# Performance work log

Hardware: AMD Instinct MI355X
Metric: run time of the kernel (lower is better)

## Reference

```python
import jax, jax.numpy as jnp
import numpy as np

N_STATE = 32  # SSM states per channel (S4D)


def lrelu(x):
    return jnp.where(x >= 0, x, 0.3 * x)


def conv1d(x, w, b, stride=1, pad=0, dil=1):
    # x: [B,C,L], w: [O,I,K]
    y = jax.lax.conv_general_dilated(
        x, w, (stride,), [(pad, pad)], rhs_dilation=(dil,),
        dimension_numbers=('NCH', 'OIH', 'NCH'))
    return y + b[None, :, None]


def batchnorm(x, g, b, eps=1e-5):
    # training-mode BatchNorm1d: stats over (B, L) per channel
    m = jnp.mean(x, axis=(0, 2), keepdims=True)
    v = jnp.var(x, axis=(0, 2), keepdims=True)
    return (x - m) * jax.lax.rsqrt(v + eps) * g[None, :, None] + b[None, :, None]


def s4_layer(u, log_dt, C2, D):
    # Diagonal S4 (S4D-Lin): u [B,H,L] -> y [B,H,L]; causal FFT conv + skip
    H, N = C2.shape[0], C2.shape[1]
    L = u.shape[-1]
    A = -0.5 + 1j * jnp.pi * jnp.arange(N, dtype=jnp.float32)            # [N]
    dtA = jnp.exp(log_dt)[:, None] * A[None, :]                          # [H,N]
    C = (C2[..., 0] + 1j * C2[..., 1]) * (jnp.exp(dtA) - 1.0) / A        # [H,N]
    vand = jnp.exp(dtA[:, :, None] * jnp.arange(L, dtype=jnp.float32))   # [H,N,L]
    K = 2.0 * jnp.real(jnp.einsum('hn,hnl->hl', C, vand))                # [H,L]
    uf = jnp.fft.rfft(u, n=2 * L)
    Kf = jnp.fft.rfft(K, n=2 * L)
    y = jnp.fft.irfft(uf * Kf[None], n=2 * L)[..., :L]
    return y + D[None, :, None] * u


def down_block(x, s4p, convs, g, b):
    # dilated residual inception down block: S4 then 4 stride-4 dilated convs
    x = s4_layer(x, *s4p)
    d1 = batchnorm(conv1d(x, convs[0][0], convs[0][1], 4, 1, 1), g, b)
    d2 = batchnorm(lrelu(conv1d(x, convs[1][0], convs[1][1], 4, 2, 2)), g, b)
    d3 = batchnorm(lrelu(conv1d(x, convs[2][0], convs[2][1], 4, 4, 4)), g, b)
    d4 = batchnorm(lrelu(conv1d(x, convs[3][0], convs[3][1], 4, 8, 8)), g, b)
    return jnp.concatenate([d1, d2, d3, d4], axis=1)


def setup_inputs() -> dict:
    key = jax.random.key(0)
    ks = iter(jax.random.split(key, 64))

    def nrm(shape, scale=1.0):
        return jax.random.normal(next(ks), shape, jnp.float32) * scale

    def logdt(H):
        lo, hi = np.log(0.001), np.log(0.1)
        return jax.random.uniform(next(ks), (H,), jnp.float32) * (hi - lo) + lo

    B, L, DIN = 16, 8192, 2
    inp = {}
    inp['x'] = nrm((B, L, DIN))
    inp['enc_w'] = nrm((64, DIN, 1), (1.0 / DIN) ** 0.5)
    inp['enc_b'] = jnp.zeros((64,), jnp.float32)
    for pfx, H in (('s4a', 64), ('s4b', 256), ('s4c', 1024)):
        inp[pfx + '_log_dt'] = logdt(H)
        inp[pfx + '_C'] = nrm((H, N_STATE, 2), 0.5 ** 0.5)
        inp[pfx + '_D'] = nrm((H,))
    for blk, C in (('b1', 64), ('b2', 256)):
        sc = (1.0 / (C * 3)) ** 0.5
        for i in range(1, 5):
            inp[f'{blk}_w{i}'] = nrm((C, C, 3), sc)
            inp[f'{blk}_b{i}'] = nrm((C,), 0.02)
    inp['bn1_g'] = jnp.ones((64,), jnp.float32)
    inp['bn1_b'] = jnp.zeros((64,), jnp.float32)
    inp['bn2_g'] = jnp.ones((256,), jnp.float32)
    inp['bn2_b'] = jnp.zeros((256,), jnp.float32)
    inp['dec1_w'] = nrm((256, 1024, 1), (1.0 / 1024) ** 0.5)
    inp['dec1_b'] = jnp.zeros((256,), jnp.float32)
    inp['dec2_w'] = nrm((1, 256, 1), (1.0 / 256) ** 0.5)
    inp['dec2_b'] = jnp.zeros((1,), jnp.float32)
    return inp


def reference(x, enc_w, enc_b,
              s4a_log_dt, s4a_C, s4a_D,
              b1_w1, b1_b1, b1_w2, b1_b2, b1_w3, b1_b3, b1_w4, b1_b4, bn1_g, bn1_b,
              s4b_log_dt, s4b_C, s4b_D,
              b2_w1, b2_b1, b2_w2, b2_b2, b2_w3, b2_b3, b2_w4, b2_b4, bn2_g, bn2_b,
              s4c_log_dt, s4c_C, s4c_D,
              dec1_w, dec1_b, dec2_w, dec2_b):
    h = conv1d(jnp.transpose(x, (0, 2, 1)), enc_w, enc_b)                 # [B,64,L]
    x1 = down_block(h, (s4a_log_dt, s4a_C, s4a_D),
                    [(b1_w1, b1_b1), (b1_w2, b1_b2), (b1_w3, b1_b3), (b1_w4, b1_b4)],
                    bn1_g, bn1_b)                                          # [B,256,L/4]
    x2 = down_block(x1, (s4b_log_dt, s4b_C, s4b_D),
                    [(b2_w1, b2_b1), (b2_w2, b2_b2), (b2_w3, b2_b3), (b2_w4, b2_b4)],
                    bn2_g, bn2_b)                                          # [B,1024,L/16]
    x3 = s4_layer(x2, s4c_log_dt, s4c_C, s4c_D)
    y = conv1d(conv1d(x3, dec1_w, dec1_b), dec2_w, dec2_b)                 # [B,1,L/16]
    ff = jnp.squeeze(y, axis=1)                                            # [B,L/16]
    return ff[..., -1:]                                                    # [B,1]
```

## Files before the change

kernel.cpp:

```cpp
#include <hip/hip_runtime.h>
#include <math.h>

#define PI_F 3.14159265358979323846f

typedef __attribute__((ext_vector_type(8))) short short8;
typedef __attribute__((ext_vector_type(4))) float f32x4;

__device__ __forceinline__ unsigned short f2bf(float f) {
    unsigned int u = __float_as_uint(f);
    unsigned int r = (u + 0x7fffu + ((u >> 16) & 1u)) >> 16;
    return (unsigned short)r;
}
__device__ __forceinline__ float bf2f(unsigned short v) {
    return __uint_as_float((unsigned int)v << 16);
}

__global__ __launch_bounds__(128) void prep_all(
    const float* __restrict__ ldt_a, const float* __restrict__ C2_a,
    const float* __restrict__ Dv_a,
    unsigned short* __restrict__ TA_a, unsigned short* __restrict__ VA_a,
    float* __restrict__ rs_a, float* __restrict__ Vrs_a,
    const float* __restrict__ ldt_b, const float* __restrict__ C2_b,
    const float* __restrict__ Dv_b,
    unsigned short* __restrict__ TA_b, unsigned short* __restrict__ VA_b,
    float* __restrict__ rs_b, float* __restrict__ Vrs_b,
    const float* __restrict__ w0, const float* __restrict__ w1,
    const float* __restrict__ w2, const float* __restrict__ w3,
    const float* __restrict__ w4, const float* __restrict__ w5,
    const float* __restrict__ w6, const float* __restrict__ w7,
    unsigned short* __restrict__ wprep)
{
    int bid = blockIdx.x, t = threadIdx.x;
    if (bid >= 320) {
        const float* wsrc[8] = {w0, w1, w2, w3, w4, w5, w6, w7};
        int e0 = (bid - 320) * 256 + t;
#pragma unroll
        for (int half = 0; half < 2; half++) {
            int e = e0 + half * 128;
            if (e < 835584) {
                int id; int doff; int Cin;
                if (e < 49152) { id = e / 12288; doff = id * 12288; Cin = 64; }
                else { id = 4 + (e - 49152) / 196608; doff = 49152 + (id - 4) * 196608; Cin = 256; }
                int el = e - doff;
                int kb = el / (Cin * 32);
                int rem = el - kb * (Cin * 32);
                int o = rem >> 5, kk = rem & 31;
                int cch = kb / 6, t6 = kb % 6, k = t6 >> 1, chalf = t6 & 1;
                int c = cch * 64 + chalf * 32 + kk;
                wprep[e] = f2bf(wsrc[id][((size_t)o * Cin + c) * 3 + k]);
            }
        }
        return;
    }
    const float* log_dt; const float* C2; const float* Dv;
    unsigned short* TA; unsigned short* VA; float* rs; float* Vrs; int h;
    if (bid < 64) { h = bid;      log_dt = ldt_a; C2 = C2_a; Dv = Dv_a; TA = TA_a; VA = VA_a; rs = rs_a; Vrs = Vrs_a; }
    else          { h = bid - 64; log_dt = ldt_b; C2 = C2_b; Dv = Dv_b; TA = TA_b; VA = VA_b; rs = rs_b; Vrs = Vrs_b; }
    __shared__ float cn[64];
    __shared__ float sK[128];
    __shared__ unsigned short s_w[128 * 66];
    float dt = expf(log_dt[h]);
    if (t < 32) {
        int n = t;
        float e = expf(-0.5f*dt);
        float s_, c_; sincosf(PI_F*dt*n, &s_, &c_);
        float wr = e*c_, wi = e*s_;
        float ar = -0.5f, ai = PI_F*n;
        float den = 1.f/(ar*ar + ai*ai);
        float tr = wr - 1.f, ti = wi;
        float qr = (tr*ar + ti*ai)*den;
        float qi = (ti*ar - tr*ai)*den;
        float c2r = C2[((size_t)h*32+n)*2], c2i = C2[((size_t)h*32+n)*2+1];
        cn[2*n]   = 2.f*(c2r*qr - c2i*qi);
        cn[2*n+1] = 2.f*(c2r*qi + c2i*qr);
        float e128 = expf(-64.f*dt);
        float s2, c2v; sincosf(PI_F*dt*n*128.f, &s2, &c2v);
        float pr = 1.f - e128*c2v, pim = -e128*s2;
        float dr = 1.f - wr, di = -wi;
        float dd = 1.f/(dr*dr + di*di);
        Vrs[(size_t)h*64 + 2*n]   = (pr*dr + pim*di)*dd;
        Vrs[(size_t)h*64 + 2*n+1] = (pim*dr - pr*di)*dd;
    }
    __syncthreads();
    {
        float em = expf(-0.5f*dt*t);
        float Kt = 0.f;
        for (int n = 0; n < 32; n++) {
            float s_, c_; sincosf(PI_F*dt*(float)(n*t), &s_, &c_);
            Kt += cn[2*n]*em*c_ - cn[2*n+1]*em*s_;
        }
        sK[t] = Kt + (t == 0 ? Dv[h] : 0.f);
    }
    if (t < 64) {
        int n = t >> 1, ri = t & 1;
        float e = expf(-0.5f*dt);
        float s_, c_; sincosf(PI_F*dt*n, &s_, &c_);
        float wr = e*c_, wi = e*s_;
        float crn = cn[2*n], cin = cn[2*n+1];
        float pr = wr, pim = wi;
        for (int m = 0; m < 128; m++) {
            float re = crn*pr - cin*pim;
            float im = crn*pim + cin*pr;
            s_w[m*66 + t] = f2bf(ri ? -im : re);
            float nr = pr*wr - pim*wi;
            float ni = pr*wi + pim*wr;
            pr = nr; pim = ni;
        }
    } else {
        int r = t - 64; int n = r >> 1, ri = r & 1;
        float e = expf(-0.5f*dt);
        float s_, c_; sincosf(PI_F*dt*n, &s_, &c_);
        float wr = e*c_, wi = e*s_;
        float cr2 = 1.f, ci2 = 0.f;
        for (int kb = 3; kb >= 0; kb--) {
            unsigned short buf[32];
            for (int kk = 31; kk >= 0; kk--) {
                buf[kk] = f2bf(ri ? ci2 : cr2);
                float nr = cr2*wr - ci2*wi;
                float ni = cr2*wi + ci2*wr;
                cr2 = nr; ci2 = ni;
            }
            uint4* dst = (uint4*)&VA[(((size_t)h*4 + kb)*64 + r)*32];
            uint4* src = (uint4*)buf;
            dst[0]=src[0]; dst[1]=src[1]; dst[2]=src[2]; dst[3]=src[3];
        }
    }
    __syncthreads();
    {
        float acc = 0.f;
        for (int tau = 0; tau <= t; tau++) acc += sK[tau];
        rs[(size_t)h*128 + t] = acc;
    }
    for (int kb = 0; kb < 4; kb++) {
        unsigned short tb[32];
#pragma unroll
        for (int kk = 0; kk < 32; kk++) {
            int col = kb*32 + kk;
            tb[kk] = f2bf((col <= t) ? sK[t - col] : 0.f);
        }
        uint4* dst = (uint4*)&TA[(((size_t)h*6 + kb)*128 + t)*32];
        uint4* src = (uint4*)tb;
        dst[0]=src[0]; dst[1]=src[1]; dst[2]=src[2]; dst[3]=src[3];
    }
    for (int i = t; i < 1024; i += 128) {
        int kb = i >> 9;
        int rem = i & 511;
        int m = rem >> 2, kkg = rem & 3;
        *(uint4*)&TA[(((size_t)h*6 + 4 + kb)*128 + m)*32 + kkg*8] =
            *(const uint4*)&s_w[m*66 + kb*32 + kkg*8];
    }
}

template<int NCH, int LOGNCH, bool ENC>
__global__ __launch_bounds__(256) void s4_layer_fused(
    const unsigned short* __restrict__ u, const float* __restrict__ xg,
    const float* __restrict__ ew, const float* __restrict__ ebv,
    const unsigned short* __restrict__ VA,
    const float* __restrict__ Vrs, const unsigned short* __restrict__ TA,
    const float* __restrict__ rs, const float* __restrict__ sc,
    const float* __restrict__ sh, const float* __restrict__ log_dt,
    unsigned short* __restrict__ yout)
{
    const int L = NCH * 128;
    __shared__ unsigned short s_u[64*200];
    __shared__ unsigned short s_s[64*72];
    __shared__ float sE[64*68];
    int h = blockIdx.y;
    int tid = threadIdx.x;
    int lane = tid & 63, wid = tid >> 6;
    int nl = lane & 15, g = lane >> 4;
    int col0 = blockIdx.x * 64;
    float scv = sc ? sc[h] : 1.f;
    float shv = sh ? sh[h] : 0.f;

    if constexpr (ENC) {
        float w0e = ew[2*h], w1e = ew[2*h+1], bbe = ebv[h];
        for (int i = tid; i < 1024; i += 256) {
            int cl = i >> 4, o = i & 15;
            int col = col0 + cl; int b = col >> LOGNCH, c = col & (NCH - 1);
            const float* xp = xg + ((size_t)b*8192 + (size_t)(c*128 + o*8))*2;
            float4 a0 = *(const float4*)xp;
            float4 a1 = *(const float4*)(xp + 4);
            float4 a2 = *(const float4*)(xp + 8);
            float4 a3 = *(const float4*)(xp + 12);
            ushort4 q0, q1;
            q0.x = f2bf(fmaf(w0e, a0.x, fmaf(w1e, a0.y, bbe)));
            q0.y = f2bf(fmaf(w0e, a0.z, fmaf(w1e, a0.w, bbe)));
            q0.z = f2bf(fmaf(w0e, a1.x, fmaf(w1e, a1.y, bbe)));
            q0.w = f2bf(fmaf(w0e, a1.z, fmaf(w1e, a1.w, bbe)));
            q1.x = f2bf(fmaf(w0e, a2.x, fmaf(w1e, a2.y, bbe)));
            q1.y = f2bf(fmaf(w0e, a2.z, fmaf(w1e, a2.w, bbe)));
            q1.z = f2bf(fmaf(w0e, a3.x, fmaf(w1e, a3.y, bbe)));
            q1.w = f2bf(fmaf(w0e, a3.z, fmaf(w1e, a3.w, bbe)));
            *(ushort4*)&s_u[cl*200 + o*8]     = q0;
            *(ushort4*)&s_u[cl*200 + o*8 + 4] = q1;
        }
    } else {
        for (int i = tid; i < 1024; i += 256) {
            int cl = i >> 4, o = i & 15;
            int col = col0 + cl; int b = col >> LOGNCH, c = col & (NCH - 1);
            *(uint4*)&s_u[cl*200 + o*8] =
                *(const uint4*)&u[((size_t)h*16 + b)*L + c*128 + o*8];
        }
    }
    __syncthreads();

    {
        int cl = wid*16 + nl;
        f32x4 acc[4];
#pragma unroll
        for (int mt = 0; mt < 4; mt++) acc[mt] = (f32x4){0.f,0.f,0.f,0.f};
#pragma unroll
        for (int kb = 0; kb < 4; kb++) {
            short8 bf = *(const short8*)&s_u[cl*200 + kb*32 + g*8];
#pragma unroll
            for (int mt = 0; mt < 4; mt++) {
                short8 af = *(const short8*)(VA + (((size_t)h*4 + kb)*64 + mt*16 + nl)*32 + g*8);
                acc[mt] = __builtin_amdgcn_mfma_f32_16x16x32_bf16(af, bf, acc[mt], 0, 0, 0);
            }
        }
#pragma unroll
        for (int mt = 0; mt < 4; mt++) {
            int j0 = mt*16 + g*4;
            float4 vr = *(const float4*)(Vrs + (size_t)h*64 + j0);
            sE[cl*68 + j0 + 0] = fmaf(scv, acc[mt][0], shv*vr.x);
            sE[cl*68 + j0 + 1] = fmaf(scv, acc[mt][1], shv*vr.y);
            sE[cl*68 + j0 + 2] = fmaf(scv, acc[mt][2], shv*vr.z);
            sE[cl*68 + j0 + 3] = fmaf(scv, acc[mt][3], shv*vr.w);
        }
    }
    __syncthreads();

    constexpr int NB = 64 / NCH;
    if (tid < NB * 32) {
        int bl = tid >> 5, n = tid & 31;
        float dt = expf(log_dt[h]);
        float e = expf(-0.5f * dt);
        float s_, c_; sincosf(PI_F * dt * n, &s_, &c_);
        float Wr = e*c_, Wi = e*s_;
#pragma unroll
        for (int i = 0; i < 7; i++) { float r = Wr*Wr - Wi*Wi; float im = 2.f*Wr*Wi; Wr = r; Wi = im; }
        float Sr = 0.f, Si = 0.f;
        for (int c2 = 0; c2 < NCH; c2++) {
            float* ep = &sE[(bl*NCH + c2)*68 + 2*n];
            float er = ep[0], ei = ep[1];
            ep[0] = Sr; ep[1] = Si;
            float r  = fmaf(Wr, Sr, fmaf(-Wi, Si, er));
            float im = fmaf(Wi, Sr, fmaf( Wr, Si, ei));
            Sr = r; Si = im;
        }
    }
    __syncthreads();

    for (int i = tid*4; i < 4096; i += 1024) {
        int cl = i >> 6, j = i & 63;
        ushort4 q;
        q.x = f2bf(sE[cl*68 + j]);
        q.y = f2bf(sE[cl*68 + j+1]);
        q.z = f2bf(sE[cl*68 + j+2]);
        q.w = f2bf(sE[cl*68 + j+3]);
        *(ushort4*)&s_s[cl*72 + j] = q;
    }
    __syncthreads();

    f32x4 accT[2][4], accW[2][4];
#pragma unroll
    for (int a = 0; a < 2; a++)
#pragma unroll
        for (int j = 0; j < 4; j++) { accT[a][j] = (f32x4){0,0,0,0}; accW[a][j] = (f32x4){0,0,0,0}; }
#pragma unroll
    for (int kb = 0; kb < 4; kb++) {
        short8 bfr[4];
#pragma unroll
        for (int j = 0; j < 4; j++)
            bfr[j] = *(const short8*)&s_u[(j*16 + nl)*200 + kb*32 + g*8];
#pragma unroll
        for (int mt2 = 0; mt2 < 2; mt2++) {
            int mtile = wid*2 + mt2;
            short8 af = *(const short8*)&TA[(((size_t)h*6 + kb)*128 + mtile*16 + nl)*32 + g*8];
#pragma unroll
            for (int j = 0; j < 4; j++)
                accT[mt2][j] = __builtin_amdgcn_mfma_f32_16x16x32_bf16(af, bfr[j], accT[mt2][j], 0, 0, 0);
        }
    }
#pragma unroll
    for (int kw = 0; kw < 2; kw++) {
        short8 bfr[4];
#pragma unroll
        for (int j = 0; j < 4; j++)
            bfr[j] = *(const short8*)&s_s[(j*16 + nl)*72 + kw*32 + g*8];
#pragma unroll
        for (int mt2 = 0; mt2 < 2; mt2++) {
            int mtile = wid*2 + mt2;
            short8 af = *(const short8*)&TA[(((size_t)h*6 + 4 + kw)*128 + mtile*16 + nl)*32 + g*8];
#pragma unroll
            for (int j = 0; j < 4; j++)
                accW[mt2][j] = __builtin_amdgcn_mfma_f32_16x16x32_bf16(af, bfr[j], accW[mt2][j], 0, 0, 0);
        }
    }
#pragma unroll
    for (int mt2 = 0; mt2 < 2; mt2++) {
        int m0 = (wid*2 + mt2)*16 + g*4;
        float4 rsv = *(const float4*)&rs[(size_t)h*128 + m0];
#pragma unroll
        for (int j = 0; j < 4; j++) {
            int col = col0 + j*16 + nl; int b = col >> LOGNCH, c = col & (NCH - 1);
            ushort4 q;
            q.x = f2bf(fmaf(scv, accT[mt2][j][0], shv*rsv.x) + accW[mt2][j][0]);
            q.y = f2bf(fmaf(scv, accT[mt2][j][1], shv*rsv.y) + accW[mt2][j][1]);
            q.z = f2bf(fmaf(scv, accT[mt2][j][2], shv*rsv.z) + accW[mt2][j][2]);
            q.w = f2bf(fmaf(scv, accT[mt2][j][3], shv*rsv.w) + accW[mt2][j][3]);
            *(ushort4*)&yout[((size_t)h*16 + b)*L + c*128 + m0] = q;
        }
    }
}

template<int CIN, int TBLK>
__global__ __launch_bounds__(256, 2) void conv_mfma4(
    const unsigned short* __restrict__ u, const unsigned short* __restrict__ wp,
    const float* __restrict__ bs0, const float* __restrict__ bs1,
    const float* __restrict__ bs2, const float* __restrict__ bs3,
    unsigned short* __restrict__ out, int Lin, int Lout)
{
    constexpr int F     = TBLK / 16;
    constexpr int NPOS  = TBLK * 4 + 16;
    constexpr int Q     = NPOS / 4;
    constexpr int NITEM = (NPOS / 8) * 64;
    constexpr int NLD   = (NITEM + 255) / 256;
    constexpr int NCC   = CIN / 64;
    constexpr int NBUF  = (NCC > 1) ? 2 : 1;
    constexpr int BUFSZ = 4 * Q * 64;
    __shared__ unsigned short s_in[NBUF * BUFSZ];

    int tid = threadIdx.x;
    int lane = tid & 63, wid = tid >> 6;
    int nl = lane & 15, g = lane >> 4;
    int t0 = blockIdx.x * TBLK;
    int b  = blockIdx.y;
    int og = blockIdx.z * 64;
    const int P0 = t0 * 4 - 8;
    const int DIL = 1 << wid;

    f32x4 acc[4][F];
#pragma unroll
    for (int m = 0; m < 4; m++)
#pragma unroll
        for (int f = 0; f < F; f++) acc[m][f] = (f32x4){0.f,0.f,0.f,0.f};

    uint4 stg[NLD];

    auto stage_load = [&](int ccbase) {
#pragma unroll
        for (int j = 0; j < NLD; j++) {
            int i = tid + 256 * j;
            uint4 v; v.x = 0u; v.y = 0u; v.z = 0u; v.w = 0u;
            if (i < NITEM) {
                int ch = i & 63, po = i >> 6;
                int p = P0 + po * 8;
                const unsigned short* gp = u + ((size_t)(ccbase + ch)*16 + b)*Lin;
                if (p >= 0 && p + 8 <= Lin) {
                    v = *(const uint4*)(gp + p);
                } else {
                    alignas(16) unsigned short t8[8];
#pragma unroll
                    for (int j2 = 0; j2 < 8; j2++) {
                        int pj = p + j2;
                        t8[j2] = ((unsigned)pj < (unsigned)Lin) ? gp[pj] : (unsigned short)0;
                    }
                    v = *(const uint4*)t8;
                }
            }
            stg[j] = v;
        }
    };
    auto stage_write = [&](int bufidx) {
        unsigned short* sb = s_in + bufidx * BUFSZ;
#pragma unroll
        for (int j = 0; j < NLD; j++) {
            int i = tid + 256 * j;
            if (i < NITEM) {
                int ch = i & 63, po = i >> 6;
                alignas(16) unsigned short t8[8];
                *(uint4*)t8 = stg[j];
#pragma unroll
                for (int jj = 0; jj < 8; jj++) {
                    int pl = po * 8 + jj;
                    int row = (pl & 3) * Q + (pl >> 2);
                    sb[row * 64 + (ch ^ ((row & 7) << 3))] = t8[jj];
                }
            }
        }
    };

    stage_load(0);
    stage_write(0);
    __syncthreads();

#pragma unroll
    for (int cc = 0; cc < NCC; cc++) {
        if (cc + 1 < NCC) stage_load((cc + 1) * 64);
        const unsigned short* sb = s_in + (NBUF > 1 ? (cc & 1) * BUFSZ : 0);
#pragma unroll
        for (int k = 0; k < 3; ++k) {
            const int off = (k - 1) * DIL + 8;
            const int r = off & 3, s = off >> 2;
#pragma unroll
            for (int chalf = 0; chalf < 2; ++chalf) {
                int kb = cc * 6 + k * 2 + chalf;
                short8 bfr[F];
#pragma unroll
                for (int f = 0; f < F; ++f) {
                    int q = f*16 + nl + s;
                    int row = r * Q + q;
                    bfr[f] = *(const short8*)&sb[row * 64 +
                        ((((chalf << 2) | g) ^ (row & 7)) << 3)];
                }
#pragma unroll
                for (int m = 0; m < 4; ++m) {
                    short8 afrag = *(const short8*)&wp[(size_t)wid*(3*CIN*CIN) +
                        ((size_t)kb*CIN + og + m*16 + nl)*32 + g*8];
#pragma unroll
                    for (int f = 0; f < F; ++f)
                        acc[m][f] = __builtin_amdgcn_mfma_f32_16x16x32_bf16(afrag, bfr[f], acc[m][f], 0, 0, 0);
                }
            }
        }
        if (cc + 1 < NCC) {
            __syncthreads();
            stage_write((cc + 1) & 1);
            __syncthreads();
        }
    }

    const float* bp = (wid == 0) ? bs0 : (wid == 1) ? bs1 : (wid == 2) ? bs2 : bs3;
#pragma unroll
    for (int m = 0; m < 4; ++m) {
#pragma unroll
        for (int f = 0; f < F; ++f) {
            int t = t0 + f*16 + nl;
#pragma unroll
            for (int r2 = 0; r2 < 4; ++r2) {
                int o = og + m*16 + g*4 + r2;
                float v = acc[m][f][r2] + bp[o];
                if (wid) v = v >= 0.f ? v : 0.3f*v;
                out[((size_t)(wid*CIN + o)*16 + b)*Lout + t] = f2bf(v);
            }
        }
    }
}

__global__ __launch_bounds__(256) void bn_stats(
    const unsigned short* __restrict__ x, const float* __restrict__ g,
    const float* __restrict__ bb, float* __restrict__ sc, float* __restrict__ sh,
    int n, int gmask)
{
    int ch = blockIdx.x;
    const unsigned short* xp = x + (size_t)ch * n;
    float s1 = 0.f, s2 = 0.f;
    for (int i = threadIdx.x*8; i < n; i += 2048) {
        uint4 raw = *(const uint4*)(xp + i);
        unsigned short us[8]; *(uint4*)us = raw;
#pragma unroll
        for (int j = 0; j < 8; j++) {
            float v = bf2f(us[j]);
            s1 += v; s2 += v*v;
        }
    }
    for (int o = 32; o > 0; o >>= 1) { s1 += __shfl_down(s1, o); s2 += __shfl_down(s2, o); }
    __shared__ float p1[4], p2[4];
    int wid = threadIdx.x >> 6;
    if ((threadIdx.x & 63) == 0) { p1[wid] = s1; p2[wid] = s2; }
    __syncthreads();
    if (threadIdx.x == 0) {
        s1 = p1[0] + p1[1] + p1[2] + p1[3];
        s2 = p2[0] + p2[1] + p2[2] + p2[3];
        float m = s1 / n;
        float var = s2 / n - m*m;
        float rstd = rsqrtf(var + 1e-5f);
        float scale = g[ch & gmask] * rstd;
        sc[ch] = scale;
        sh[ch] = fmaf(-m, scale, bb[ch & gmask]);
    }
}

__global__ __launch_bounds__(256) void s4c_all(
    const unsigned short* __restrict__ u,
    const float* __restrict__ sc, const float* __restrict__ sh,
    const float* __restrict__ log_dt, const float* __restrict__ C2,
    const float* __restrict__ Dv, float* __restrict__ x3last)
{
    __shared__ float sE[64 * 68];
    __shared__ float red[16 * 33];
    __shared__ unsigned short sVA[4 * 64 * 32];
    __shared__ alignas(16) float sVrs[64];
    int h = blockIdx.x;
    int tid = threadIdx.x;
    int lane = tid & 63, wid = tid >> 6;
    int nl = lane & 15, g = lane >> 4;
    float scv = sc[h], shv = sh[h];
    float dt = expf(log_dt[h]);

    {
        int t = lane, n = t >> 1, ri = t & 1;
        int kb = wid;
        float e = expf(-0.5f*dt);
        float s_, c_; sincosf(PI_F*dt*n, &s_, &c_);
        float wr = e*c_, wi = e*s_;
        int e0 = 96 - kb*32;
        float em0 = expf(-0.5f*dt*(float)e0);
        float s0, c0; sincosf(PI_F*dt*(float)n*(float)e0, &s0, &c0);
        float cr2 = em0*c0, ci2 = em0*s0;
        alignas(16) unsigned short buf[32];
        for (int kk = 31; kk >= 0; kk--) {
            buf[kk] = f2bf(ri ? ci2 : cr2);
            float nr = cr2*wr - ci2*wi;
            float ni = cr2*wi + ci2*wr;
            cr2 = nr; ci2 = ni;
        }
        int key = (t >> 1) & 3;
        uint4* dst = (uint4*)&sVA[(kb*64 + t)*32];
        uint4* src4 = (uint4*)buf;
#pragma unroll
        for (int cc = 0; cc < 4; cc++) dst[cc ^ key] = src4[cc];
        if (wid == 0 && ri == 0) {
            float e128 = expf(-64.f*dt);
            float s2, c2v; sincosf(PI_F*dt*n*128.f, &s2, &c2v);
            float pr = 1.f - e128*c2v, pim = -e128*s2;
            float dr = 1.f - wr, di = -wi;
            float dd = 1.f/(dr*dr + di*di);
            sVrs[2*n]   = (pr*dr + pim*di)*dd;
            sVrs[2*n+1] = (pim*dr - pr*di)*dd;
        }
    }
    __syncthreads();

    int rkey = (nl >> 1) & 3;
    {
        int col = wid*16 + nl;
        int b = col >> 2, c = col & 3;
        const unsigned short* up = u + ((size_t)h*16 + b)*512 + c*128;
        f32x4 acc[4];
#pragma unroll
        for (int mt = 0; mt < 4; mt++) acc[mt] = (f32x4){0.f,0.f,0.f,0.f};
#pragma unroll
        for (int kb = 0; kb < 4; kb++) {
            short8 bf = *(const short8*)(up + kb*32 + g*8);
#pragma unroll
            for (int mt = 0; mt < 4; mt++) {
                short8 af = *(const short8*)&sVA[(kb*64 + mt*16 + nl)*32 + ((g ^ rkey) << 3)];
                acc[mt] = __builtin_amdgcn_mfma_f32_16x16x32_bf16(af, bf, acc[mt], 0, 0, 0);
            }
        }
#pragma unroll
        for (int mt = 0; mt < 4; mt++) {
            int j0 = mt*16 + g*4;
            float4 vr = *(const float4*)&sVrs[j0];
            sE[col*68 + j0 + 0] = fmaf(scv, acc[mt][0], shv*vr.x);
            sE[col*68 + j0 + 1] = fmaf(scv, acc[mt][1], shv*vr.y);
            sE[col*68 + j0 + 2] = fmaf(scv, acc[mt][2], shv*vr.z);
            sE[col*68 + j0 + 3] = fmaf(scv, acc[mt][3], shv*vr.w);
        }
    }
    __syncthreads();

    if (tid < 64) {
        int n = lane >> 1, bh = lane & 1;
        float e = expf(-0.5f * dt);
        float s_, c_; sincosf(PI_F * dt * n, &s_, &c_);
        float wr = e*c_, wi = e*s_;
        float ar = -0.5f, ai = PI_F * n;
        float den = 1.f / (ar*ar + ai*ai);
        float tr = wr - 1.f, ti = wi;
        float qr = (tr*ar + ti*ai) * den;
        float qi = (ti*ar - tr*ai) * den;
        float c2r = C2[((size_t)h*32 + n)*2], c2i = C2[((size_t)h*32 + n)*2 + 1];
        float crv = c2r*qr - c2i*qi, civ = c2r*qi + c2i*qr;
        float Wr = wr, Wi = wi;
#pragma unroll
        for (int i = 0; i < 7; i++) { float r = Wr*Wr - Wi*Wi; float im = 2.f*Wr*Wi; Wr = r; Wi = im; }
#pragma unroll
        for (int b2 = 0; b2 < 8; b2++) {
            int b = bh*8 + b2;
            float Sr = 0.f, Si = 0.f;
#pragma unroll
            for (int c = 0; c < 4; c++) {
                int col = b*4 + c;
                float er = sE[col*68 + 2*n], ei = sE[col*68 + 2*n + 1];
                float r  = fmaf(Wr, Sr, fmaf(-Wi, Si, er));
                float im = fmaf(Wi, Sr, fmaf( Wr, Si, ei));
                Sr = r; Si = im;
            }
            red[b*33 + n] = crv*Sr - civ*Si;
        }
    }
    __syncthreads();
    if (tid < 16) {
        int b = tid;
        float s = 0.f;
        for (int n2 = 0; n2 < 32; n2++) s += red[b*33 + n2];
        float uv = fmaf(scv, bf2f(u[((size_t)h*16 + b)*512 + 511]), shv);
        x3last[b*1024 + h] = 2.f*s + Dv[h]*uv;
    }
}

__global__ __launch_bounds__(256) void dec_kernel(
    const float* __restrict__ x3last, const float* __restrict__ w1, const float* __restrict__ b1,
    const float* __restrict__ w2, const float* __restrict__ b2, float* __restrict__ out)
{
    __shared__ float xs[1024];
    int b = blockIdx.x, tid = threadIdx.x;
    for (int i = tid; i < 1024; i += 256) xs[i] = x3last[b*1024 + i];
    __syncthreads();
    float z = b1[tid];
    const float* wpt = w1 + (size_t)tid*1024;
    for (int i = 0; i < 1024; i += 4) {
        float4 wv = *(const float4*)(wpt + i);
        z = fmaf(wv.x, xs[i],   z);
        z = fmaf(wv.y, xs[i+1], z);
        z = fmaf(wv.z, xs[i+2], z);
        z = fmaf(wv.w, xs[i+3], z);
    }
    float v = w2[tid] * z;
    for (int o = 32; o > 0; o >>= 1) v += __shfl_down(v, o);
    __shared__ float ps[4];
    if ((tid & 63) == 0) ps[tid >> 6] = v;
    __syncthreads();
    if (tid == 0) out[b] = ps[0] + ps[1] + ps[2] + ps[3] + b2[0];
}

extern "C" void kernel_launch(void* const* d_in, const int* in_sizes, int n_in,
                              void* d_out, int out_size, void* d_ws, size_t ws_size,
                              hipStream_t stream)
{
    const float* x       = (const float*)d_in[0];
    const float* enc_w   = (const float*)d_in[1];
    const float* enc_b   = (const float*)d_in[2];
    const float* s4a_ldt = (const float*)d_in[3];
    const float* s4a_C   = (const float*)d_in[4];
    const float* s4a_D   = (const float*)d_in[5];
    const float* s4b_ldt = (const float*)d_in[6];
    const float* s4b_C   = (const float*)d_in[7];
    const float* s4b_D   = (const float*)d_in[8];
    const float* s4c_ldt = (const float*)d_in[9];
    const float* s4c_C   = (const float*)d_in[10];
    const float* s4c_D   = (const float*)d_in[11];
    const float* b1w[4] = {(const float*)d_in[12], (const float*)d_in[14], (const float*)d_in[16], (const float*)d_in[18]};
    const float* b1b[4] = {(const float*)d_in[13], (const float*)d_in[15], (const float*)d_in[17], (const float*)d_in[19]};
    const float* b2w[4] = {(const float*)d_in[20], (const float*)d_in[22], (const float*)d_in[24], (const float*)d_in[26]};
    const float* b2b[4] = {(const float*)d_in[21], (const float*)d_in[23], (const float*)d_in[25], (const float*)d_in[27]};
    const float* bn1_g  = (const float*)d_in[28];
    const float* bn1_b  = (const float*)d_in[29];
    const float* bn2_g  = (const float*)d_in[30];
    const float* bn2_b  = (const float*)d_in[31];
    const float* dec1_w = (const float*)d_in[32];
    const float* dec1_b = (const float*)d_in[33];
    const float* dec2_w = (const float*)d_in[34];
    const float* dec2_b = (const float*)d_in[35];
    float* out = (float*)d_out;

    char* ws = (char*)d_ws;
    unsigned short* u3    = (unsigned short*)(ws);
    unsigned short* ya    = (unsigned short*)(ws + 16777216);
    unsigned short* yb    = ya;
    unsigned short* u2    = (unsigned short*)(ws + 33554432);
    unsigned short* wprep = (unsigned short*)(ws + 88080384);
    unsigned short* TA_a  = (unsigned short*)(ws + 89751552);
    unsigned short* TA_b  = (unsigned short*)(ws + 92897280);
    unsigned short* VA_a  = (unsigned short*)(ws + 105480192);
    unsigned short* VA_b  = (unsigned short*)(ws + 106528768);
    float*          rs_a  = (float*)(ws + 110723072);
    float*          rs_b  = (float*)(ws + 110755840);
    float*          Vrs_a = (float*)(ws + 110886912);
    float*          Vrs_b = (float*)(ws + 110903296);
    float*          smallp= (float*)(ws + 110968832);
    float* sc1 = smallp;
    float* sh1 = smallp + 256;
    float* sc2 = smallp + 512;
    float* sh2 = smallp + 1536;
    float* x3l = smallp + 2560;

    prep_all<<<3584, 128, 0, stream>>>(
        s4a_ldt, s4a_C, s4a_D, TA_a, VA_a, rs_a, Vrs_a,
        s4b_ldt, s4b_C, s4b_D, TA_b, VA_b, rs_b, Vrs_b,
        b1w[0], b1w[1], b1w[2], b1w[3], b2w[0], b2w[1], b2w[2], b2w[3], wprep);

    s4_layer_fused<64,6,true><<<dim3(16, 64), 256, 0, stream>>>(
        nullptr, x, enc_w, enc_b, VA_a, Vrs_a, TA_a, rs_a, nullptr, nullptr, s4a_ldt, ya);

    conv_mfma4<64,32><<<dim3(64, 16, 1), 256, 0, stream>>>(
        ya, wprep, b1b[0], b1b[1], b1b[2], b1b[3], u2, 8192, 2048);
    bn_stats<<<256, 256, 0, stream>>>(u2, bn1_g, bn1_b, sc1, sh1, 16*2048, 63);

    s4_layer_fused<16,4,false><<<dim3(4, 256), 256, 0, stream>>>(
        u2, nullptr, nullptr, nullptr, VA_b, Vrs_b, TA_b, rs_b, sc1, sh1, s4b_ldt, yb);

    conv_mfma4<256,64><<<dim3(8, 16, 4), 256, 0, stream>>>(
        yb, wprep + 49152, b2b[0], b2b[1], b2b[2], b2b[3], u3, 2048, 512);
    bn_stats<<<1024, 256, 0, stream>>>(u3, bn2_g, bn2_b, sc2, sh2, 16*512, 255);

    s4c_all<<<1024, 256, 0, stream>>>(u3, sc2, sh2, s4c_ldt, s4c_C, s4c_D, x3l);

    dec_kernel<<<16, 256, 0, stream>>>(x3l, dec1_w, dec1_b, dec2_w, dec2_b, out);
}
```

Measured before the change: 296.6 us.

## Fuse batchnorm statistics into conv epilogue via atomics, drop bn_stats kernels

```diff
diff --git a/kernel.cpp b/kernel.cpp
--- a/kernel.cpp
+++ b/kernel.cpp
@@ -28,10 +28,12 @@
     const float* __restrict__ w2, const float* __restrict__ w3,
     const float* __restrict__ w4, const float* __restrict__ w5,
     const float* __restrict__ w6, const float* __restrict__ w7,
-    unsigned short* __restrict__ wprep)
+    unsigned short* __restrict__ wprep, float* __restrict__ bnsum)
 {
     int bid = blockIdx.x, t = threadIdx.x;
     if (bid >= 320) {
+        int z = (bid - 320) * 128 + t;
+        if (z < 20480) bnsum[z] = 0.f;
         const float* wsrc[8] = {w0, w1, w2, w3, w4, w5, w6, w7};
         int e0 = (bid - 320) * 256 + t;
 #pragma unroll
@@ -151,14 +153,16 @@
     }
 }
 
-template<int NCH, int LOGNCH, bool ENC>
+template<int NCH, int LOGNCH, bool ENC, bool BN>
 __global__ __launch_bounds__(256) void s4_layer_fused(
     const unsigned short* __restrict__ u, const float* __restrict__ xg,
     const float* __restrict__ ew, const float* __restrict__ ebv,
     const unsigned short* __restrict__ VA,
     const float* __restrict__ Vrs, const unsigned short* __restrict__ TA,
-    const float* __restrict__ rs, const float* __restrict__ sc,
-    const float* __restrict__ sh, const float* __restrict__ log_dt,
+    const float* __restrict__ rs,
+    const float* __restrict__ bnsum, const float* __restrict__ bng,
+    const float* __restrict__ bnb, int bnC, int bnN, int gmask,
+    const float* __restrict__ log_dt,
     unsigned short* __restrict__ yout)
 {
     const int L = NCH * 128;
@@ -170,8 +174,20 @@
     int lane = tid & 63, wid = tid >> 6;
     int nl = lane & 15, g = lane >> 4;
     int col0 = blockIdx.x * 64;
-    float scv = sc ? sc[h] : 1.f;
-    float shv = sh ? sh[h] : 0.f;
+    float scv = 1.f, shv = 0.f;
+    if constexpr (BN) {
+        float s1 = 0.f, s2 = 0.f;
+#pragma unroll
+        for (int k = 0; k < 8; k++) {
+            s1 += bnsum[((size_t)k*bnC + h)*2];
+            s2 += bnsum[((size_t)k*bnC + h)*2 + 1];
+        }
+        float m = s1 / (float)bnN;
+        float var = s2 / (float)bnN - m*m;
+        float rstd = rsqrtf(var + 1e-5f);
+        scv = bng[h & gmask] * rstd;
+        shv = fmaf(-m, scv, bnb[h & gmask]);
+    }
 
     if constexpr (ENC) {
         float w0e = ew[2*h], w1e = ew[2*h+1], bbe = ebv[h];
@@ -320,7 +336,8 @@
     const unsigned short* __restrict__ u, const unsigned short* __restrict__ wp,
     const float* __restrict__ bs0, const float* __restrict__ bs1,
     const float* __restrict__ bs2, const float* __restrict__ bs3,
-    unsigned short* __restrict__ out, int Lin, int Lout)
+    unsigned short* __restrict__ out, float* __restrict__ bnacc,
+    int Lin, int Lout)
 {
     constexpr int F     = TBLK / 16;
     constexpr int NPOS  = TBLK * 4 + 16;
@@ -447,45 +464,39 @@
             }
         }
     }
-}
-
-__global__ __launch_bounds__(256) void bn_stats(
-    const unsigned short* __restrict__ x, const float* __restrict__ g,
-    const float* __restrict__ bb, float* __restrict__ sc, float* __restrict__ sh,
-    int n, int gmask)
-{
-    int ch = blockIdx.x;
-    const unsigned short* xp = x + (size_t)ch * n;
-    float s1 = 0.f, s2 = 0.f;
-    for (int i = threadIdx.x*8; i < n; i += 2048) {
-        uint4 raw = *(const uint4*)(xp + i);
-        unsigned short us[8]; *(uint4*)us = raw;
-#pragma unroll
-        for (int j = 0; j < 8; j++) {
-            float v = bf2f(us[j]);
-            s1 += v; s2 += v*v;
-        }
-    }
-    for (int o = 32; o > 0; o >>= 1) { s1 += __shfl_down(s1, o); s2 += __shfl_down(s2, o); }
-    __shared__ float p1[4], p2[4];
-    int wid = threadIdx.x >> 6;
-    if ((threadIdx.x & 63) == 0) { p1[wid] = s1; p2[wid] = s2; }
-    __syncthreads();
-    if (threadIdx.x == 0) {
-        s1 = p1[0] + p1[1] + p1[2] + p1[3];
-        s2 = p2[0] + p2[1] + p2[2] + p2[3];
-        float m = s1 / n;
-        float var = s2 / n - m*m;
-        float rstd = rsqrtf(var + 1e-5f);
-        float scale = g[ch & gmask] * rstd;
-        sc[ch] = scale;
-        sh[ch] = fmaf(-m, scale, bb[ch & gmask]);
+
+    float* bacc = bnacc + (size_t)(blockIdx.x & 7) * (4*CIN) * 2;
+#pragma unroll
+    for (int m = 0; m < 4; ++m) {
+#pragma unroll
+        for (int r2 = 0; r2 < 4; ++r2) {
+            int o = og + m*16 + g*4 + r2;
+            float bv = bp[o];
+            float s = 0.f, ss = 0.f;
+#pragma unroll
+            for (int f = 0; f < F; ++f) {
+                float v = acc[m][f][r2] + bv;
+                if (wid) v = v >= 0.f ? v : 0.3f*v;
+                s += v; ss += v*v;
+            }
+#pragma unroll
+            for (int off2 = 1; off2 < 16; off2 <<= 1) {
+                s  += __shfl_xor(s, off2);
+                ss += __shfl_xor(ss, off2);
+            }
+            if (nl == 0) {
+                int ch = wid*CIN + o;
+                atomicAdd(&bacc[ch*2],     s);
+                atomicAdd(&bacc[ch*2 + 1], ss);
+            }
+        }
     }
 }
 
 __global__ __launch_bounds__(256) void s4c_all(
     const unsigned short* __restrict__ u,
-    const float* __restrict__ sc, const float* __restrict__ sh,
+    const float* __restrict__ bnsum, const float* __restrict__ bng,
+    const float* __restrict__ bnb,
     const float* __restrict__ log_dt, const float* __restrict__ C2,
     const float* __restrict__ Dv, float* __restrict__ x3last)
 {
@@ -497,8 +508,21 @@
     int tid = threadIdx.x;
     int lane = tid & 63, wid = tid >> 6;
     int nl = lane & 15, g = lane >> 4;
-    float scv = sc[h], shv = sh[h];
     float dt = expf(log_dt[h]);
+    float scv, shv;
+    {
+        float s1 = 0.f, s2 = 0.f;
+#pragma unroll
+        for (int k = 0; k < 8; k++) {
+            s1 += bnsum[((size_t)k*1024 + h)*2];
+            s2 += bnsum[((size_t)k*1024 + h)*2 + 1];
+        }
+        float m = s1 / 8192.f;
+        float var = s2 / 8192.f - m*m;
+        float rstd = rsqrtf(var + 1e-5f);
+        scv = bng[h & 255] * rstd;
+        shv = fmaf(-m, scv, bnb[h & 255]);
+    }
 
     {
         int t = lane, n = t >> 1, ri = t & 1;
@@ -673,32 +697,31 @@
     float*          Vrs_a = (float*)(ws + 110886912);
     float*          Vrs_b = (float*)(ws + 110903296);
     float*          smallp= (float*)(ws + 110968832);
-    float* sc1 = smallp;
-    float* sh1 = smallp + 256;
-    float* sc2 = smallp + 512;
-    float* sh2 = smallp + 1536;
-    float* x3l = smallp + 2560;
+    float* bsum1 = smallp;
+    float* bsum2 = smallp + 4096;
+    float* x3l   = smallp + 20480;
 
     prep_all<<<3584, 128, 0, stream>>>(
         s4a_ldt, s4a_C, s4a_D, TA_a, VA_a, rs_a, Vrs_a,
         s4b_ldt, s4b_C, s4b_D, TA_b, VA_b, rs_b, Vrs_b,
-        b1w[0], b1w[1], b1w[2], b1w[3], b2w[0], b2w[1], b2w[2], b2w[3], wprep);
-
-    s4_layer_fused<64,6,true><<<dim3(16, 64), 256, 0, stream>>>(
-        nullptr, x, enc_w, enc_b, VA_a, Vrs_a, TA_a, rs_a, nullptr, nullptr, s4a_ldt, ya);
+        b1w[0], b1w[1], b1w[2], b1w[3], b2w[0], b2w[1], b2w[2], b2w[3],
+        wprep, bsum1);
+
+    s4_layer_fused<64,6,true,false><<<dim3(16, 64), 256, 0, stream>>>(
+        nullptr, x, enc_w, enc_b, VA_a, Vrs_a, TA_a, rs_a,
+        nullptr, nullptr, nullptr, 0, 0, 0, s4a_ldt, ya);
 
     conv_mfma4<64,32><<<dim3(64, 16, 1), 256, 0, stream>>>(
-        ya, wprep, b1b[0], b1b[1], b1b[2], b1b[3], u2, 8192, 2048);
-    bn_stats<<<256, 256, 0, stream>>>(u2, bn1_g, bn1_b, sc1, sh1, 16*2048, 63);
-
-    s4_layer_fused<16,4,false><<<dim3(4, 256), 256, 0, stream>>>(
-        u2, nullptr, nullptr, nullptr, VA_b, Vrs_b, TA_b, rs_b, sc1, sh1, s4b_ldt, yb);
+        ya, wprep, b1b[0], b1b[1], b1b[2], b1b[3], u2, bsum1, 8192, 2048);
+
+    s4_layer_fused<16,4,false,true><<<dim3(4, 256), 256, 0, stream>>>(
+        u2, nullptr, nullptr, nullptr, VA_b, Vrs_b, TA_b, rs_b,
+        bsum1, bn1_g, bn1_b, 256, 32768, 63, s4b_ldt, yb);
 
     conv_mfma4<256,64><<<dim3(8, 16, 4), 256, 0, stream>>>(
-        yb, wprep + 49152, b2b[0], b2b[1], b2b[2], b2b[3], u3, 2048, 512);
-    bn_stats<<<1024, 256, 0, stream>>>(u3, bn2_g, bn2_b, sc2, sh2, 16*512, 255);
-
-    s4c_all<<<1024, 256, 0, stream>>>(u3, sc2, sh2, s4c_ldt, s4c_C, s4c_D, x3l);
+        yb, wprep + 49152, b2b[0], b2b[1], b2b[2], b2b[3], u3, bsum2, 2048, 512);
+
+    s4c_all<<<1024, 256, 0, stream>>>(u3, bsum2, bn2_g, bn2_b, s4c_ldt, s4c_C, s4c_D, x3l);
 
     dec_kernel<<<16, 256, 0, stream>>>(x3l, dec1_w, dec1_b, dec2_w, dec2_b, out);
 }
```

After: 337.9 us. 13.9% more time.
